# Kernel optimization log

Hardware: AMD Instinct MI355X
Metric: run time of the kernel (lower is better)

The kernel has to match this reference:

```python
import jax, jax.numpy as jnp
import numpy as np

N_NODES = 50000
N_EDGES = 800000
NODE_IN = 256
EDGE_IN = 64
HEADS = 8
OUT = 16
HID = HEADS * OUT  # 128
EPS = 1e-5


def layernorm(x, g, b):
    mu = jnp.mean(x, axis=-1, keepdims=True)
    var = jnp.var(x, axis=-1, keepdims=True)
    return (x - mu) * jax.lax.rsqrt(var + EPS) * g + b


def setup_inputs() -> dict:
    key = jax.random.key(0)
    ks = jax.random.split(key, 12)
    node_feats = jax.random.normal(ks[0], (N_NODES, NODE_IN), dtype=jnp.float32)
    edge_feats = jax.random.normal(ks[1], (N_EDGES, EDGE_IN), dtype=jnp.float32)
    src = jax.random.randint(ks[2], (N_EDGES,), 0, N_NODES)
    dst = jax.random.randint(ks[3], (N_EDGES,), 0, N_NODES)
    W_node = jax.random.normal(ks[4], (NODE_IN, HID), dtype=jnp.float32) / np.sqrt(NODE_IN)
    g_node = jnp.ones((HID,), jnp.float32)
    b_node = jnp.zeros((HID,), jnp.float32)
    W_edge = jax.random.normal(ks[5], (EDGE_IN, HID), dtype=jnp.float32) / np.sqrt(EDGE_IN)
    g_edge = jnp.ones((HID,), jnp.float32)
    b_edge = jnp.zeros((HID,), jnp.float32)
    W_out = jax.random.normal(ks[6], (HID, OUT), dtype=jnp.float32) / np.sqrt(HID)
    g_out = jnp.ones((OUT,), jnp.float32)
    b_out = jnp.zeros((OUT,), jnp.float32)
    return {
        'node_feats': node_feats, 'edge_feats': edge_feats, 'src': src, 'dst': dst,
        'W_node': W_node, 'g_node': g_node, 'b_node': b_node,
        'W_edge': W_edge, 'g_edge': g_edge, 'b_edge': b_edge,
        'W_out': W_out, 'g_out': g_out, 'b_out': b_out,
    }


def reference(node_feats, edge_feats, src, dst,
              W_node, g_node, b_node,
              W_edge, g_edge, b_edge,
              W_out, g_out, b_out):
    # project_node: Linear(no bias) -> GELU (exact) -> LayerNorm
    hv = layernorm(jax.nn.gelu(node_feats @ W_node, approximate=False), g_node, b_node)  # [N, HID]
    # project_edge: Linear(no bias) -> LayerNorm, then exp
    he = jnp.exp(layernorm(edge_feats @ W_edge, g_edge, b_edge))  # [E, HID]
    # u_mul_e then sum to dst (head structure is elementwise, so keep flat HID)
    msgs = hv[src] * he  # [E, HID]
    h = jax.ops.segment_sum(msgs, dst, num_segments=N_NODES)  # [N, HID]
    # project_out: Linear(no bias) -> GELU -> LayerNorm
    return layernorm(jax.nn.gelu(h @ W_out, approximate=False), g_out, b_out)  # [N, OUT]
```

## Files before the change

kernel.cpp:

```cpp
#include <hip/hip_runtime.h>

#define N_NODES 50000
#define N_EDGES 800000
#define NODE_IN 256
#define EDGE_IN 64
#define HID 128
#define OUTD 16
#define LN_EPS 1e-5f

typedef __attribute__((ext_vector_type(4))) float f32x4;
typedef __attribute__((ext_vector_type(8))) _Float16 half8;
typedef __attribute__((ext_vector_type(4))) _Float16 half4;

__device__ __forceinline__ float gelu_exact(float x) {
    return 0.5f * x * (1.0f + erff(x * 0.70710678118654752f));
}

__global__ __launch_bounds__(256) void zero_kernel(int4* __restrict__ p, int n4) {
    int i = blockIdx.x * 256 + threadIdx.x;
    const int stride = gridDim.x * 256;
    for (; i < n4; i += stride) p[i] = make_int4(0, 0, 0, 0);
}

__global__ void setup_kernel(const float* __restrict__ Wn, const float* __restrict__ We,
                             _Float16* __restrict__ WTn, _Float16* __restrict__ WTe) {
    int t = blockIdx.x * blockDim.x + threadIdx.x;
    int stride = gridDim.x * blockDim.x;
    for (int i = t; i < HID * NODE_IN; i += stride) {
        int n = i >> 8, k = i & 255;
        WTn[i] = (_Float16)Wn[k * HID + n];
    }
    for (int i = t; i < HID * EDGE_IN; i += stride) {
        int n = i >> 6, k = i & 63;
        WTe[i] = (_Float16)We[k * HID + n];
    }
}

__global__ __launch_bounds__(256) void count_kernel(const int* __restrict__ dst,
                                                    int* __restrict__ tot) {
    int e = blockIdx.x * 256 + threadIdx.x;
    if (e < N_EDGES) atomicAdd(&tot[dst[e]], 1);
}

__global__ __launch_bounds__(256) void scan1_kernel(const int* __restrict__ tot,
                                                    int* __restrict__ offs,
                                                    int* __restrict__ btot) {
    __shared__ int lsum[256];
    const int t = threadIdx.x;
    const int base = blockIdx.x * 1024 + t * 4;
    int v[4]; int s = 0;
    #pragma unroll
    for (int j = 0; j < 4; ++j) {
        int idx = base + j;
        v[j] = (idx < N_NODES) ? tot[idx] : 0;
        s += v[j];
    }
    lsum[t] = s;
    __syncthreads();
    for (int d = 1; d < 256; d <<= 1) {
        int x = (t >= d) ? lsum[t - d] : 0;
        __syncthreads();
        lsum[t] += x;
        __syncthreads();
    }
    int excl = lsum[t] - s;
    if (t == 255) btot[blockIdx.x] = lsum[255];
    int run = excl;
    #pragma unroll
    for (int j = 0; j < 4; ++j) {
        int idx = base + j;
        if (idx < N_NODES) offs[idx] = run;
        run += v[j];
    }
}

__global__ __launch_bounds__(256) void scan2_kernel(int* __restrict__ offs,
                                                    const int* __restrict__ btot,
                                                    int* __restrict__ cur) {
    int s = 0;
    for (int i = 0; i < (int)blockIdx.x; ++i) s += btot[i];
    const int t = threadIdx.x;
    const int base = blockIdx.x * 1024 + t * 4;
    #pragma unroll
    for (int j = 0; j < 4; ++j) {
        int idx = base + j;
        if (idx < N_NODES) {
            int v = offs[idx] + s;
            offs[idx] = v;
            cur[idx] = v;
        }
    }
    if (blockIdx.x == 0 && t == 0) offs[N_NODES] = N_EDGES;
}

__global__ __launch_bounds__(256) void place2_kernel(const int* __restrict__ src,
                                                     const int* __restrict__ dst,
                                                     int* __restrict__ cur,
                                                     int* __restrict__ perm,
                                                     int* __restrict__ psrc,
                                                     int* __restrict__ pdst) {
    int e = blockIdx.x * 256 + threadIdx.x;
    if (e < N_EDGES) {
        const int d = dst[e];
        const int pos = atomicAdd(&cur[d], 1);
        perm[pos] = e;
        psrc[pos] = src[e];
        pdst[pos] = d;
    }
}

__global__ __launch_bounds__(256) void node_kernel(
    const float* __restrict__ X,
    const _Float16* __restrict__ WT,
    const float* __restrict__ g, const float* __restrict__ b,
    _Float16* __restrict__ hv)
{
    __shared__ __align__(16) _Float16 lA[64 * 72];
    __shared__ __align__(16) _Float16 lB[128 * 72];

    const int t = threadIdx.x;
    const int wave = t >> 6, lane = t & 63;
    const int x15 = lane & 15, quad = lane >> 4;
    const int row0 = blockIdx.x * 64;

    float gc[8], bc[8];
    #pragma unroll
    for (int c = 0; c < 8; ++c) { gc[c] = g[16 * c + x15]; bc[c] = b[16 * c + x15]; }

    f32x4 acc[8];
    #pragma unroll
    for (int c = 0; c < 8; ++c) acc[c] = (f32x4)(0.0f);

    for (int kc = 0; kc < 4; ++kc) {
        const int k0 = kc * 64;
        __syncthreads();
        #pragma unroll
        for (int j = 0; j < 4; ++j) {
            int idx = j * 1024 + t * 4;
            int r = idx >> 6, kk = idx & 63;
            int grow = row0 + r;
            float4 v = make_float4(0.f, 0.f, 0.f, 0.f);
            if (grow < N_NODES) v = *(const float4*)(X + grow * NODE_IN + k0 + kk);
            half4 h4;
            h4[0] = (_Float16)v.x; h4[1] = (_Float16)v.y;
            h4[2] = (_Float16)v.z; h4[3] = (_Float16)v.w;
            *(half4*)(lA + r * 72 + kk) = h4;
        }
        #pragma unroll
        for (int j = 0; j < 4; ++j) {
            int idx = j * 2048 + t * 8;
            int n = idx >> 6, kk = idx & 63;
            half8 v = *(const half8*)(WT + n * NODE_IN + k0 + kk);
            *(half8*)(lB + n * 72 + kk) = v;
        }
        __syncthreads();
        #pragma unroll
        for (int ks = 0; ks < 2; ++ks) {
            half8 a = *(const half8*)(lA + (wave * 16 + x15) * 72 + ks * 32 + quad * 8);
            #pragma unroll
            for (int c = 0; c < 8; ++c) {
                half8 bb = *(const half8*)(lB + (c * 16 + x15) * 72 + ks * 32 + quad * 8);
                acc[c] = __builtin_amdgcn_mfma_f32_16x16x32_f16(a, bb, acc[c], 0, 0, 0);
            }
        }
    }

    float v[8][4], s[4], sq[4];
    #pragma unroll
    for (int r = 0; r < 4; ++r) { s[r] = 0.f; sq[r] = 0.f; }
    #pragma unroll
    for (int c = 0; c < 8; ++c)
        #pragma unroll
        for (int r = 0; r < 4; ++r) {
            float x = gelu_exact(acc[c][r]);
            v[c][r] = x; s[r] += x; sq[r] += x * x;
        }
    #pragma unroll
    for (int m = 1; m <= 8; m <<= 1)
        #pragma unroll
        for (int r = 0; r < 4; ++r) {
            s[r]  += __shfl_xor(s[r],  m, 64);
            sq[r] += __shfl_xor(sq[r], m, 64);
        }
    #pragma unroll
    for (int r = 0; r < 4; ++r) {
        int row = row0 + wave * 16 + quad * 4 + r;
        if (row >= N_NODES) continue;
        float mean = s[r] * (1.f / 128.f);
        float var  = sq[r] * (1.f / 128.f) - mean * mean;
        float rstd = rsqrtf(var + LN_EPS);
        half8 o;
        #pragma unroll
        for (int c = 0; c < 8; ++c)
            o[c] = (_Float16)((v[c][r] - mean) * rstd * gc[c] + bc[c]);
        *(half8*)(hv + row * HID + x15 * 8) = o;
    }
}

__global__ __launch_bounds__(256) void fagg_kernel(
    const float* __restrict__ EF,
    const int* __restrict__ perm, const int* __restrict__ psrc,
    const int* __restrict__ pdst, const int* __restrict__ offs,
    const _Float16* __restrict__ WT,
    const float* __restrict__ g, const float* __restrict__ b,
    const _Float16* __restrict__ hv,
    long long* __restrict__ h64)
{
    __shared__ __align__(16) _Float16 lA[64 * 72];
    __shared__ __align__(16) float lprod[64 * 128];
    __shared__ int lperm[64];
    __shared__ int lsrc[64];
    __shared__ int ldst[64];

    const int t = threadIdx.x;
    const int wave = t >> 6, lane = t & 63;
    const int x15 = lane & 15, quad = lane >> 4;
    const int base = blockIdx.x * 64;

    half8 Bf[8][2];
    #pragma unroll
    for (int c = 0; c < 8; ++c)
        #pragma unroll
        for (int ks = 0; ks < 2; ++ks)
            Bf[c][ks] = *(const half8*)(WT + (c * 16 + x15) * EDGE_IN + ks * 32 + quad * 8);

    float gc[8], bc[8];
    #pragma unroll
    for (int c = 0; c < 8; ++c) { gc[c] = g[16 * c + x15]; bc[c] = b[16 * c + x15]; }

    if (t < 64)            lperm[t]       = perm[base + t];
    else if (t < 128)      lsrc[t - 64]   = psrc[base + t - 64];
    else if (t < 192)      ldst[t - 128]  = pdst[base + t - 128];
    __syncthreads();

    #pragma unroll
    for (int j = 0; j < 4; ++j) {
        int idx = j * 1024 + t * 4;
        int r = idx >> 6, kk = idx & 63;
        const float4 v = *(const float4*)(EF + (size_t)lperm[r] * EDGE_IN + kk);
        half4 h4;
        h4[0] = (_Float16)v.x; h4[1] = (_Float16)v.y;
        h4[2] = (_Float16)v.z; h4[3] = (_Float16)v.w;
        *(half4*)(lA + r * 72 + kk) = h4;
    }
    __syncthreads();

    f32x4 acc[8];
    #pragma unroll
    for (int c = 0; c < 8; ++c) acc[c] = (f32x4)(0.0f);
    #pragma unroll
    for (int ks = 0; ks < 2; ++ks) {
        half8 a = *(const half8*)(lA + (wave * 16 + x15) * 72 + ks * 32 + quad * 8);
        #pragma unroll
        for (int c = 0; c < 8; ++c)
            acc[c] = __builtin_amdgcn_mfma_f32_16x16x32_f16(a, Bf[c][ks], acc[c], 0, 0, 0);
    }

    float s[4], sq[4];
    #pragma unroll
    for (int r = 0; r < 4; ++r) { s[r] = 0.f; sq[r] = 0.f; }
    #pragma unroll
    for (int c = 0; c < 8; ++c)
        #pragma unroll
        for (int r = 0; r < 4; ++r) { float x = acc[c][r]; s[r] += x; sq[r] += x * x; }
    #pragma unroll
    for (int m = 1; m <= 8; m <<= 1)
        #pragma unroll
        for (int r = 0; r < 4; ++r) {
            s[r]  += __shfl_xor(s[r],  m, 64);
            sq[r] += __shfl_xor(sq[r], m, 64);
        }

    #pragma unroll
    for (int r = 0; r < 4; ++r) {
        const int erow = wave * 16 + quad * 4 + r;
        const int se = lsrc[erow];
        const half8 hg = *(const half8*)(hv + (size_t)se * HID + x15 * 8);
        float mean = s[r] * (1.f / 128.f);
        float var  = sq[r] * (1.f / 128.f) - mean * mean;
        float rstd = rsqrtf(var + LN_EPS);
        f32x4 p0, p1;
        #pragma unroll
        for (int c = 0; c < 8; ++c) {
            float he = __expf((acc[c][r] - mean) * rstd * gc[c] + bc[c]);
            float pr = he * (float)hg[c];
            if (c < 4) p0[c] = pr; else p1[c - 4] = pr;
        }
        float* lp = lprod + erow * 128 + x15 * 8;
        *(f32x4*)lp = p0;
        *(f32x4*)(lp + 4) = p1;
    }
    __syncthreads();

    if (t < 128) {
        const int j = t;
        long long run = 0;
        int rs = 0;
        for (int r = 0; r < 64; ++r) {
            run += llrintf(lprod[r * 128 + j] * 4294967296.0f);
            const bool close = (r == 63) || (ldst[r + 1] != ldst[r]);
            if (close) {
                const int d = ldst[r];
                const int segbeg = offs[d], segend = offs[d + 1];
                long long* hp = h64 + (size_t)d * HID + j;
                if (segbeg == base + rs && segend == base + r + 1) {
                    *hp = run;
                } else {
                    atomicAdd((unsigned long long*)hp, (unsigned long long)run);
                }
                run = 0; rs = r + 1;
            }
        }
    }
}

__global__ __launch_bounds__(256) void out_kernel(
    const long long* __restrict__ h64,
    const float* __restrict__ W,
    const float* __restrict__ g, const float* __restrict__ b,
    float* __restrict__ out)
{
    __shared__ float lW[HID * OUTD];
    __shared__ float lh[16][HID];
    const int t = threadIdx.x;
    const int node0 = blockIdx.x * 16;

    for (int i = t; i < HID * OUTD; i += 256) lW[i] = W[i];
    for (int i = t; i < 16 * HID; i += 256) {
        int row = i >> 7, p = i & 127;
        int k = 16 * (p & 7) + (p >> 3);
        int grow = node0 + row;
        lh[row][k] = (grow < N_NODES)
                   ? (float)h64[(size_t)grow * HID + p] * 0x1p-32f
                   : 0.f;
    }
    __syncthreads();

    const int i = t >> 4, j = t & 15;
    float acc = 0.f;
    #pragma unroll 8
    for (int k = 0; k < HID; ++k)
        acc = fmaf(lh[i][k], lW[k * OUTD + j], acc);
    float x = gelu_exact(acc);
    float s = x, sq = x * x;
    #pragma unroll
    for (int m = 1; m <= 8; m <<= 1) {
        s  += __shfl_xor(s,  m, 64);
        sq += __shfl_xor(sq, m, 64);
    }
    float mean = s * (1.f / 16.f);
    float var  = sq * (1.f / 16.f) - mean * mean;
    float rstd = rsqrtf(var + LN_EPS);
    int grow = node0 + i;
    if (grow < N_NODES) out[grow * OUTD + j] = (x - mean) * rstd * g[j] + b[j];
}

extern "C" void kernel_launch(void* const* d_in, const int* in_sizes, int n_in,
                              void* d_out, int out_size, void* d_ws, size_t ws_size,
                              hipStream_t stream) {
    const float* node_feats = (const float*)d_in[0];
    const float* edge_feats = (const float*)d_in[1];
    const int*   src        = (const int*)d_in[2];
    const int*   dst        = (const int*)d_in[3];
    const float* W_node     = (const float*)d_in[4];
    const float* g_node     = (const float*)d_in[5];
    const float* b_node     = (const float*)d_in[6];
    const float* W_edge     = (const float*)d_in[7];
    const float* g_edge     = (const float*)d_in[8];
    const float* b_edge     = (const float*)d_in[9];
    const float* W_out      = (const float*)d_in[10];
    const float* g_out      = (const float*)d_in[11];
    const float* b_out      = (const float*)d_in[12];
    float* out = (float*)d_out;

    char* ws = (char*)d_ws;
    size_t o = 0;
    _Float16* hv  = (_Float16*)(ws + o); o += (size_t)N_NODES * HID * 2;
    _Float16* WTn = (_Float16*)(ws + o); o += (size_t)HID * NODE_IN * 2;
    _Float16* WTe = (_Float16*)(ws + o); o += (size_t)HID * EDGE_IN * 2;
    int* tot  = (int*)(ws + o); o += (size_t)N_NODES * 4;
    int* offs = (int*)(ws + o); o += (size_t)(N_NODES + 16) * 4;
    int* btot = (int*)(ws + o); o += 1024;
    int* cur  = (int*)(ws + o); o += (size_t)N_NODES * 4;
    int* perm = (int*)(ws + o); o += (size_t)N_EDGES * 4;
    int* psrc = (int*)(ws + o); o += (size_t)N_EDGES * 4;
    int* pdst = (int*)(ws + o); o += (size_t)N_EDGES * 4;
    o = (o + 511) & ~(size_t)511;
    long long* h64 = (long long*)(ws + o);

    zero_kernel<<<49, 256, 0, stream>>>((int4*)tot, N_NODES / 4);
    setup_kernel<<<128, 256, 0, stream>>>(W_node, W_edge, WTn, WTe);
    node_kernel<<<(N_NODES + 63) / 64, 256, 0, stream>>>(node_feats, WTn, g_node, b_node, hv);
    count_kernel<<<N_EDGES / 256, 256, 0, stream>>>(dst, tot);
    scan1_kernel<<<49, 256, 0, stream>>>(tot, offs, btot);
    scan2_kernel<<<49, 256, 0, stream>>>(offs, btot, cur);
    place2_kernel<<<N_EDGES / 256, 256, 0, stream>>>(src, dst, cur, perm, psrc, pdst);
    zero_kernel<<<2048, 256, 0, stream>>>((int4*)h64, (int)((size_t)N_NODES * HID * 8 / 16));
    fagg_kernel<<<N_EDGES / 64, 256, 0, stream>>>(edge_feats, perm, psrc, pdst, offs,
                                                  WTe, g_edge, b_edge, hv, h64);
    out_kernel<<<(N_NODES + 15) / 16, 256, 0, stream>>>(h64, W_out, g_out, b_out, out);
}
```

Baseline: 678.6 us.

## Replace serial per-column segment scan with per-segment LDS atomic accumulation

The old tail wrote all 64x128 edge products to shared memory, then 128 threads walked the 64 rows serially, accumulating runs per destination. Now each thread accumulates fixed-point products in registers across its 4 rows, flushes closed segments into a small per-segment LDS accumulator via 64-bit shared atomics, and the whole block writes segment results out in parallel. A wave-level prefix scan computes segment ids and boundaries, with a fallback to global atomics when a tile has more than 16 segments. This removes the long serial scan and shrinks LDS use, in exchange for 64-bit LDS atomic traffic and extra setup work.

```diff
diff --git a/kernel.cpp b/kernel.cpp
--- a/kernel.cpp
+++ b/kernel.cpp
@@ -197,6 +197,8 @@
     }
 }
 
+#define NSMAX 16
+
 __global__ __launch_bounds__(256) void fagg_kernel(
     const float* __restrict__ EF,
     const int* __restrict__ perm, const int* __restrict__ psrc,
@@ -207,10 +209,14 @@
     long long* __restrict__ h64)
 {
     __shared__ __align__(16) _Float16 lA[64 * 72];
-    __shared__ __align__(16) float lprod[64 * 128];
+    __shared__ unsigned long long lacc[NSMAX * 128];
     __shared__ int lperm[64];
     __shared__ int lsrc[64];
     __shared__ int ldst[64];
+    __shared__ int lseg[64];
+    __shared__ int lsegfr[NSMAX];
+    __shared__ int lseglr[NSMAX];
+    __shared__ int lnseg;
 
     const int t = threadIdx.x;
     const int wave = t >> 6, lane = t & 63;
@@ -228,9 +234,13 @@
     #pragma unroll
     for (int c = 0; c < 8; ++c) { gc[c] = g[16 * c + x15]; bc[c] = b[16 * c + x15]; }
 
-    if (t < 64)            lperm[t]       = perm[base + t];
-    else if (t < 128)      lsrc[t - 64]   = psrc[base + t - 64];
-    else if (t < 192)      ldst[t - 128]  = pdst[base + t - 128];
+    if (t < 64) {
+        lperm[t] = perm[base + t];
+        lsrc[t]  = psrc[base + t];
+        ldst[t]  = pdst[base + t];
+    } else {
+        for (int i = t - 64; i < NSMAX * 128; i += 192) lacc[i] = 0ull;
+    }
     __syncthreads();
 
     #pragma unroll
@@ -243,7 +253,24 @@
         h4[2] = (_Float16)v.z; h4[3] = (_Float16)v.w;
         *(half4*)(lA + r * 72 + kk) = h4;
     }
+    if (t < 64) {
+        const int bnd = (t > 0 && ldst[t] != ldst[t - 1]) ? 1 : 0;
+        int sc = bnd;
+        #pragma unroll
+        for (int m = 1; m < 64; m <<= 1) {
+            int o = __shfl_up(sc, m, 64);
+            if (t >= m) sc += o;
+        }
+        lseg[t] = sc;
+        if (sc < NSMAX) {
+            if (bnd || t == 0) lsegfr[sc] = t;
+            if (t == 63 || ldst[t + 1] != ldst[t]) lseglr[sc] = t;
+        }
+        if (t == 63) lnseg = sc + 1;
+    }
     __syncthreads();
+
+    const int nsg = lnseg;
 
     f32x4 acc[8];
     #pragma unroll
@@ -271,45 +298,55 @@
             sq[r] += __shfl_xor(sq[r], m, 64);
         }
 
-    #pragma unroll
-    for (int r = 0; r < 4; ++r) {
-        const int erow = wave * 16 + quad * 4 + r;
+    long long a8[8];
+    #pragma unroll
+    for (int c = 0; c < 8; ++c) a8[c] = 0;
+
+    #pragma unroll
+    for (int rr = 0; rr < 4; ++rr) {
+        const int erow = wave * 16 + quad * 4 + rr;
         const int se = lsrc[erow];
         const half8 hg = *(const half8*)(hv + (size_t)se * HID + x15 * 8);
-        float mean = s[r] * (1.f / 128.f);
-        float var  = sq[r] * (1.f / 128.f) - mean * mean;
-        float rstd = rsqrtf(var + LN_EPS);
-        f32x4 p0, p1;
+        const float mean = s[rr] * (1.f / 128.f);
+        const float var  = sq[rr] * (1.f / 128.f) - mean * mean;
+        const float rstd = rsqrtf(var + LN_EPS);
         #pragma unroll
         for (int c = 0; c < 8; ++c) {
-            float he = __expf((acc[c][r] - mean) * rstd * gc[c] + bc[c]);
-            float pr = he * (float)hg[c];
-            if (c < 4) p0[c] = pr; else p1[c - 4] = pr;
-        }
-        float* lp = lprod + erow * 128 + x15 * 8;
-        *(f32x4*)lp = p0;
-        *(f32x4*)(lp + 4) = p1;
+            const float he = __expf((acc[c][rr] - mean) * rstd * gc[c] + bc[c]);
+            const float pr = he * (float)hg[c];
+            a8[c] += llrintf(pr * 4294967296.0f);
+        }
+        const int dcur = ldst[erow];
+        const bool close = (rr == 3) || (ldst[erow + 1] != dcur);
+        if (close) {
+            if (nsg <= NSMAX) {
+                const int sgi = lseg[erow];
+                unsigned long long* lp = &lacc[sgi * 128 + x15 * 8];
+                #pragma unroll
+                for (int c = 0; c < 8; ++c)
+                    atomicAdd(&lp[c], (unsigned long long)a8[c]);
+            } else {
+                long long* hp = h64 + (size_t)dcur * HID + x15 * 8;
+                #pragma unroll
+                for (int c = 0; c < 8; ++c)
+                    atomicAdd((unsigned long long*)&hp[c], (unsigned long long)a8[c]);
+            }
+            #pragma unroll
+            for (int c = 0; c < 8; ++c) a8[c] = 0;
+        }
     }
     __syncthreads();
 
-    if (t < 128) {
-        const int j = t;
-        long long run = 0;
-        int rs = 0;
-        for (int r = 0; r < 64; ++r) {
-            run += llrintf(lprod[r * 128 + j] * 4294967296.0f);
-            const bool close = (r == 63) || (ldst[r + 1] != ldst[r]);
-            if (close) {
-                const int d = ldst[r];
-                const int segbeg = offs[d], segend = offs[d + 1];
-                long long* hp = h64 + (size_t)d * HID + j;
-                if (segbeg == base + rs && segend == base + r + 1) {
-                    *hp = run;
-                } else {
-                    atomicAdd((unsigned long long*)hp, (unsigned long long)run);
-                }
-                run = 0; rs = r + 1;
-            }
+    if (nsg <= NSMAX) {
+        const int tot = nsg * 128;
+        for (int i = t; i < tot; i += 256) {
+            const int sgi = i >> 7, col = i & 127;
+            const int fr = lsegfr[sgi], lr = lseglr[sgi];
+            const int d = ldst[fr];
+            const long long v = (long long)lacc[sgi * 128 + col];
+            long long* hp = h64 + (size_t)d * HID + col;
+            if (offs[d] == base + fr && offs[d + 1] == base + lr + 1) *hp = v;
+            else atomicAdd((unsigned long long*)hp, (unsigned long long)v);
         }
     }
 }
```

Measured after the change: 632.4 us. 6.8% less time.

## Pad CSR segments to multiples of four edges for per-lane pre-reduction in fagg

Applied to the files above, without the earlier changes.

Each destination's edge segment is rounded up to a multiple of four slots, with padded slots marked by src=-1 and filled by new prefill and padfill kernels. Because every group of four rows now belongs to one destination, each lane can sum its four rows' fixed-point products in registers. This shrinks the shared-memory staging buffer and makes the serial scan over 64 rows a scan over 16 groups. The cost is up to about 3N extra padded edges processed as wasted MFMA work, plus two extra kernel launches and extra memory fills.

```diff
diff --git a/kernel.cpp b/kernel.cpp
--- a/kernel.cpp
+++ b/kernel.cpp
@@ -7,6 +7,7 @@
 #define HID 128
 #define OUTD 16
 #define LN_EPS 1e-5f
+#define CAPE (((N_EDGES + 3 * N_NODES) + 63) & ~63)
 
 typedef __attribute__((ext_vector_type(4))) float f32x4;
 typedef __attribute__((ext_vector_type(8))) _Float16 half8;
@@ -52,7 +53,7 @@
     #pragma unroll
     for (int j = 0; j < 4; ++j) {
         int idx = base + j;
-        v[j] = (idx < N_NODES) ? tot[idx] : 0;
+        v[j] = (idx < N_NODES) ? ((tot[idx] + 3) & ~3) : 0;
         s += v[j];
     }
     lsum[t] = s;
@@ -90,7 +91,25 @@
             cur[idx] = v;
         }
     }
-    if (blockIdx.x == 0 && t == 0) offs[N_NODES] = N_EDGES;
+    if (blockIdx.x == gridDim.x - 1 && t == 0)
+        offs[N_NODES] = s + btot[blockIdx.x];
+}
+
+__global__ __launch_bounds__(256) void prefill_kernel(int* __restrict__ perm,
+                                                      int* __restrict__ psrc,
+                                                      int* __restrict__ pdst) {
+    int i = blockIdx.x * 256 + threadIdx.x;
+    if (i < CAPE) { perm[i] = 0; psrc[i] = -1; pdst[i] = -1; }
+}
+
+__global__ __launch_bounds__(256) void padfill_kernel(const int* __restrict__ tot,
+                                                      const int* __restrict__ offs,
+                                                      int* __restrict__ pdst) {
+    int n = blockIdx.x * 256 + threadIdx.x;
+    if (n < N_NODES) {
+        int s = offs[n] + tot[n], e = offs[n + 1];
+        for (int p = s; p < e; ++p) pdst[p] = n;
+    }
 }
 
 __global__ __launch_bounds__(256) void place2_kernel(const int* __restrict__ src,
@@ -207,15 +226,17 @@
     long long* __restrict__ h64)
 {
     __shared__ __align__(16) _Float16 lA[64 * 72];
-    __shared__ __align__(16) float lprod[64 * 128];
+    __shared__ long long lpart[16 * 128];
     __shared__ int lperm[64];
     __shared__ int lsrc[64];
     __shared__ int ldst[64];
 
+    const int base = blockIdx.x * 64;
+    if (base >= offs[N_NODES]) return;
+
     const int t = threadIdx.x;
     const int wave = t >> 6, lane = t & 63;
     const int x15 = lane & 15, quad = lane >> 4;
-    const int base = blockIdx.x * 64;
 
     half8 Bf[8][2];
     #pragma unroll
@@ -228,9 +249,9 @@
     #pragma unroll
     for (int c = 0; c < 8; ++c) { gc[c] = g[16 * c + x15]; bc[c] = b[16 * c + x15]; }
 
-    if (t < 64)            lperm[t]       = perm[base + t];
-    else if (t < 128)      lsrc[t - 64]   = psrc[base + t - 64];
-    else if (t < 192)      ldst[t - 128]  = pdst[base + t - 128];
+    if (t < 64)       lperm[t]      = perm[base + t];
+    else if (t < 128) lsrc[t - 64]  = psrc[base + t - 64];
+    else if (t < 192) ldst[t - 128] = pdst[base + t - 128];
     __syncthreads();
 
     #pragma unroll
@@ -271,44 +292,49 @@
             sq[r] += __shfl_xor(sq[r], m, 64);
         }
 
-    #pragma unroll
-    for (int r = 0; r < 4; ++r) {
-        const int erow = wave * 16 + quad * 4 + r;
+    const int rg = wave * 4 + quad;
+    long long a8[8];
+    #pragma unroll
+    for (int c = 0; c < 8; ++c) a8[c] = 0;
+
+    #pragma unroll
+    for (int rr = 0; rr < 4; ++rr) {
+        const int erow = rg * 4 + rr;
         const int se = lsrc[erow];
-        const half8 hg = *(const half8*)(hv + (size_t)se * HID + x15 * 8);
-        float mean = s[r] * (1.f / 128.f);
-        float var  = sq[r] * (1.f / 128.f) - mean * mean;
-        float rstd = rsqrtf(var + LN_EPS);
-        f32x4 p0, p1;
-        #pragma unroll
-        for (int c = 0; c < 8; ++c) {
-            float he = __expf((acc[c][r] - mean) * rstd * gc[c] + bc[c]);
-            float pr = he * (float)hg[c];
-            if (c < 4) p0[c] = pr; else p1[c - 4] = pr;
-        }
-        float* lp = lprod + erow * 128 + x15 * 8;
-        *(f32x4*)lp = p0;
-        *(f32x4*)(lp + 4) = p1;
-    }
+        if (se >= 0) {
+            const half8 hg = *(const half8*)(hv + (size_t)se * HID + x15 * 8);
+            const float mean = s[rr] * (1.f / 128.f);
+            const float var  = sq[rr] * (1.f / 128.f) - mean * mean;
+            const float rstd = rsqrtf(var + LN_EPS);
+            #pragma unroll
+            for (int c = 0; c < 8; ++c) {
+                const float he = __expf((acc[c][rr] - mean) * rstd * gc[c] + bc[c]);
+                a8[c] += llrintf(he * (float)hg[c] * 4294967296.0f);
+            }
+        }
+    }
+    long long* lp = &lpart[rg * 128 + x15 * 8];
+    #pragma unroll
+    for (int c = 0; c < 8; ++c) lp[c] = a8[c];
     __syncthreads();
 
     if (t < 128) {
         const int j = t;
         long long run = 0;
         int rs = 0;
-        for (int r = 0; r < 64; ++r) {
-            run += llrintf(lprod[r * 128 + j] * 4294967296.0f);
-            const bool close = (r == 63) || (ldst[r + 1] != ldst[r]);
+        for (int rgw = 0; rgw < 16; ++rgw) {
+            run += lpart[rgw * 128 + j];
+            const int d = ldst[rgw * 4];
+            const bool close = (rgw == 15) || (ldst[rgw * 4 + 4] != d);
             if (close) {
-                const int d = ldst[r];
-                const int segbeg = offs[d], segend = offs[d + 1];
-                long long* hp = h64 + (size_t)d * HID + j;
-                if (segbeg == base + rs && segend == base + r + 1) {
-                    *hp = run;
-                } else {
-                    atomicAdd((unsigned long long*)hp, (unsigned long long)run);
+                if (d >= 0) {
+                    long long* hp = h64 + (size_t)d * HID + j;
+                    if (offs[d] == base + rs * 4 && offs[d + 1] == base + rgw * 4 + 4)
+                        *hp = run;
+                    else
+                        atomicAdd((unsigned long long*)hp, (unsigned long long)run);
                 }
-                run = 0; rs = r + 1;
+                run = 0; rs = rgw + 1;
             }
         }
     }
@@ -382,9 +408,9 @@
     int* offs = (int*)(ws + o); o += (size_t)(N_NODES + 16) * 4;
     int* btot = (int*)(ws + o); o += 1024;
     int* cur  = (int*)(ws + o); o += (size_t)N_NODES * 4;
-    int* perm = (int*)(ws + o); o += (size_t)N_EDGES * 4;
-    int* psrc = (int*)(ws + o); o += (size_t)N_EDGES * 4;
-    int* pdst = (int*)(ws + o); o += (size_t)N_EDGES * 4;
+    int* perm = (int*)(ws + o); o += (size_t)CAPE * 4;
+    int* psrc = (int*)(ws + o); o += (size_t)CAPE * 4;
+    int* pdst = (int*)(ws + o); o += (size_t)CAPE * 4;
     o = (o + 511) & ~(size_t)511;
     long long* h64 = (long long*)(ws + o);
 
@@ -394,9 +420,11 @@
     count_kernel<<<N_EDGES / 256, 256, 0, stream>>>(dst, tot);
     scan1_kernel<<<49, 256, 0, stream>>>(tot, offs, btot);
     scan2_kernel<<<49, 256, 0, stream>>>(offs, btot, cur);
+    prefill_kernel<<<(CAPE + 255) / 256, 256, 0, stream>>>(perm, psrc, pdst);
+    padfill_kernel<<<(N_NODES + 255) / 256, 256, 0, stream>>>(tot, offs, pdst);
     place2_kernel<<<N_EDGES / 256, 256, 0, stream>>>(src, dst, cur, perm, psrc, pdst);
     zero_kernel<<<2048, 256, 0, stream>>>((int4*)h64, (int)((size_t)N_NODES * HID * 8 / 16));
-    fagg_kernel<<<N_EDGES / 64, 256, 0, stream>>>(edge_feats, perm, psrc, pdst, offs,
-                                                  WTe, g_edge, b_edge, hv, h64);
+    fagg_kernel<<<CAPE / 64, 256, 0, stream>>>(edge_feats, perm, psrc, pdst, offs,
+                                               WTe, g_edge, b_edge, hv, h64);
     out_kernel<<<(N_NODES + 15) / 16, 256, 0, stream>>>(h64, W_out, g_out, b_out, out);
 }
```

Measured after the change: 651.5 us. 1.04x faster.
